# Kernel optimization log

Hardware: AMD Instinct MI355X
Metric: run time of the kernel (lower is better)

## Reference

```python
import jax, jax.numpy as jnp
import numpy as np

N = 50000      # nodes
E = 800000     # edges
D_IN = 128
D_H = 128
D_OUT = 64
P = 0.3        # dropout prob


def _glorot(key, out_c, in_c):
    return jax.random.normal(key, (out_c, in_c), jnp.float32) * (1.0 / np.sqrt(in_c))


def setup_inputs() -> dict:
    key = jax.random.key(0)
    ks = jax.random.split(key, 10)
    return {
        "x": jax.random.normal(ks[0], (N, D_IN), jnp.float32),
        "u1": jax.random.uniform(ks[1], (N, D_H), jnp.float32),
        "u2": jax.random.uniform(ks[2], (N, D_H), jnp.float32),
        "wl0": _glorot(ks[3], D_H, D_IN), "bl0": jnp.zeros((D_H,), jnp.float32), "wr0": _glorot(ks[4], D_H, D_IN),
        "wl1": _glorot(ks[5], D_H, D_H), "bl1": jnp.zeros((D_H,), jnp.float32), "wr1": _glorot(ks[6], D_H, D_H),
        "wl2": _glorot(ks[7], D_OUT, D_H), "bl2": jnp.zeros((D_OUT,), jnp.float32), "wr2": _glorot(ks[8], D_OUT, D_H),
        "edge_index": jax.random.randint(ks[9], (2, E), 0, N),
    }


def _sage_conv(x, src, dst, wl, bl, wr):
    # PyG SAGEConv (aggr='mean'): lin_l(mean of neighbor msgs) + lin_r(x)
    msg = x[src]                                                    # [E, d] gather
    s = jax.ops.segment_sum(msg, dst, num_segments=N)               # [N, d] scatter-sum
    cnt = jax.ops.segment_sum(jnp.ones((dst.shape[0],), x.dtype), dst, num_segments=N)
    mean = s / jnp.maximum(cnt, 1.0)[:, None]                       # mean; 0 for isolated nodes
    return mean @ wl.T + bl + x @ wr.T


def reference(x, u1, u2, wl0, bl0, wr0, wl1, bl1, wr1, wl2, bl2, wr2, edge_index):
    src, dst = edge_index[0], edge_index[1]
    keep = 1.0 - P
    h = jax.nn.relu(_sage_conv(x, src, dst, wl0, bl0, wr0))
    h = h * ((u1 >= P).astype(h.dtype) / keep)                      # dropout (training=True)
    h = jax.nn.relu(_sage_conv(h, src, dst, wl1, bl1, wr1))
    h = h * ((u2 >= P).astype(h.dtype) / keep)
    return _sage_conv(h, src, dst, wl2, bl2, wr2)
```

## Files before the change

### kernel.cpp

```cpp
#include <hip/hip_runtime.h>


constexpr int N = 50000;
constexpr int E = 800000;
constexpr int NBUCK = (N + 255) / 256;
constexpr int CE = 2048;
constexpr int NEB = (E + CE - 1) / CE;
constexpr int SLOT = 5632;
static_assert(N <= 65536, "u16 packing");
static_assert(N % 16 == 0, "16-row blocks need no bounds checks");

typedef _Float16 f16x8 __attribute__((ext_vector_type(8)));
typedef _Float16 f16x4 __attribute__((ext_vector_type(4)));
typedef _Float16 f16x2 __attribute__((ext_vector_type(2)));
typedef float f32x4 __attribute__((ext_vector_type(4)));


__global__ __launch_bounds__(256) void bucket_scatter_kernel(
    const int* __restrict__ src, const int* __restrict__ dst,
    int* __restrict__ bcur, unsigned* __restrict__ T) {
  __shared__ unsigned sorted[CE];
  __shared__ int hist[256], scan[256], excl[256], lcur[256], gbase[256];
  const int t = threadIdx.x;
  const int e0 = blockIdx.x * CE;
  const int nval = min(CE, E - e0);
  hist[t] = 0;
  __syncthreads();
  for (int i = t; i < nval; i += 256) atomicAdd(&hist[dst[e0 + i] >> 8], 1);
  __syncthreads();
  const int h = hist[t];
  scan[t] = h;
  __syncthreads();
  for (int off = 1; off < 256; off <<= 1) {
    int u = (t >= off) ? scan[t - off] : 0;
    __syncthreads();
    scan[t] += u;
    __syncthreads();
  }
  excl[t] = scan[t] - h;
  lcur[t] = scan[t] - h;
  gbase[t] = (t < NBUCK && h > 0) ? atomicAdd(&bcur[t], h) : 0;
  __syncthreads();
  for (int i = t; i < nval; i += 256) {
    int e = e0 + i;
    int d = dst[e];
    int p = atomicAdd(&lcur[d >> 8], 1);
    sorted[p] = ((unsigned)d << 16) | (unsigned)src[e];
  }
  __syncthreads();
  for (int i = t; i < nval; i += 256) {
    unsigned pk = sorted[i];
    int b = pk >> 24;
    T[gbase[b] + (i - excl[b])] = pk;
  }
}

constexpr int MASKB = (N * 128) / (8 * 256);

__global__ __launch_bounds__(256) void bucket_place_kernel(
    const unsigned* __restrict__ T, const int* __restrict__ bcur,
    const float* __restrict__ u1, const float* __restrict__ u2,
    unsigned* __restrict__ mk1, unsigned* __restrict__ mk2,
    int* __restrict__ offs, int* __restrict__ deg, int* __restrict__ elist) {
  __shared__ int dcnt[256], s[256], ncur[256];
  const int t = threadIdx.x;
  const int b = blockIdx.x;
  if (b >= NBUCK) {
    int mb = b - NBUCK;
    const float* Us = (mb < MASKB) ? u1 : u2;
    unsigned* MKs = (mb < MASKB) ? mk1 : mk2;
    int bb = (mb < MASKB) ? mb : (mb - MASKB);
#pragma unroll
    for (int k = 0; k < 8; ++k) {
      int i = (bb * 8 + k) * 256 + t;
      unsigned long long m = __ballot(Us[i] >= 0.3f);
      int lt = t & 63;
      if (lt == 0) MKs[i >> 5] = (unsigned)m;
      else if (lt == 32) MKs[i >> 5] = (unsigned)(m >> 32);
    }
    return;
  }
  const int lo = b * SLOT;
  const int hi = bcur[b];
  dcnt[t] = 0;
  __syncthreads();
  for (int i = lo + t; i < hi; i += 256) atomicAdd(&dcnt[(T[i] >> 16) & 255], 1);
  __syncthreads();
  const int v = dcnt[t];
  const int pv = (v + 3) & ~3;
  s[t] = pv;
  __syncthreads();
  for (int off = 1; off < 256; off <<= 1) {
    int u = (t >= off) ? s[t - off] : 0;
    __syncthreads();
    s[t] += u;
    __syncthreads();
  }
  const int base = lo + s[t] - pv;
  const int node = b * 256 + t;
  if (node < N) { offs[node] = base; deg[node] = v; }
  ncur[t] = base;
  __syncthreads();
  for (int i = lo + t; i < hi; i += 256) {
    unsigned pk = T[i];
    int pos = atomicAdd(&ncur[(pk >> 16) & 255], 1);
    elist[pos] = (int)(pk & 0xffffu);
  }
}

__device__ inline void wfrag_build(int idx, int KB, const float* wl,
                                   const float* wr, _Float16* wf) {
  int j = idx & 7;
  int lane = (idx >> 3) & 63;
  int kb = (idx >> 9) % KB;
  int ct = (idx >> 9) / KB;
  int c = ct * 16 + (lane & 15);
  int k = kb * 32 + (lane >> 4) * 8 + j;
  float v = (k < 128) ? wl[c * 128 + k] : wr[c * 128 + (k - 128)];
  wf[idx] = (_Float16)v;
}

constexpr int CONVB = (N * 128 / 8 + 255) / 256;

__global__ __launch_bounds__(256) void setup_kernel(
    const float* __restrict__ x,
    const float* __restrict__ wl0, const float* __restrict__ wr0,
    const float* __restrict__ wl1, const float* __restrict__ wr1,
    const float* __restrict__ wl2, const float* __restrict__ wr2,
    _Float16* __restrict__ HA, _Float16* __restrict__ wf0,
    _Float16* __restrict__ wf1, _Float16* __restrict__ wfZ,
    int* __restrict__ bcur) {
  const int b = blockIdx.x;
  const int t = threadIdx.x;
  if (b < CONVB) {
    int i = b * 256 + t;
    if (i < N * 128 / 8) {
      float4 a = ((const float4*)x)[i * 2];
      float4 c = ((const float4*)x)[i * 2 + 1];
      f16x8 v;
      v[0] = (_Float16)a.x; v[1] = (_Float16)a.y; v[2] = (_Float16)a.z; v[3] = (_Float16)a.w;
      v[4] = (_Float16)c.x; v[5] = (_Float16)c.y; v[6] = (_Float16)c.z; v[7] = (_Float16)c.w;
      ((f16x8*)HA)[i] = v;
    }
  } else if (b < CONVB + 128) {
    wfrag_build((b - CONVB) * 256 + t, 8, wl0, wr0, wf0);
  } else if (b < CONVB + 256) {
    wfrag_build((b - CONVB - 128) * 256 + t, 8, wl1, wr1, wf1);
  } else if (b < CONVB + 320) {
    int idx = (b - CONVB - 256) * 256 + t;
    int j = idx & 7;
    int lane = (idx >> 3) & 63;
    int kb = (idx >> 9) & 3;
    int ct = idx >> 11;
    int c = ct * 16 + (lane & 15);
    int k = kb * 32 + (lane >> 4) * 8 + j;
    float v = (c < 64) ? wl2[c * 128 + k] : wr2[(c - 64) * 128 + k];
    wfZ[idx] = (_Float16)v;
  } else {
    if (t < NBUCK) bcur[t] = t * SLOT;
  }
}

__global__ __launch_bounds__(256, 8) void fused_layer_kernel(
    const _Float16* __restrict__ H, const int* __restrict__ offs,
    const int* __restrict__ deg, const int* __restrict__ elist,
    const _Float16* __restrict__ Wf, const float* __restrict__ bias,
    const unsigned* __restrict__ MK, _Float16* __restrict__ outp) {
  __shared__ __align__(16) _Float16 Af[8][64][8];
  const int t = threadIdx.x;
  const int rowbase = blockIdx.x * 16;

  {
    int r = t >> 4, o = t & 15;
    f16x8 v = *(const f16x8*)(H + (size_t)(rowbase + r) * 128 + o * 8);
    *(f16x8*)&Af[4 + (o >> 2)][(o & 3) * 16 + r][0] = v;
  }

  {
    const int hw = t >> 5;
    const int ll = t & 31;
    const int kb = ll >> 3, q = (ll >> 1) & 3, j = (ll & 1) * 4;
#pragma unroll 1
    for (int i = 0; i < 2; ++i) {
      int r = hw * 2 + i;
      int node = rowbase + r;
      float a0 = 0.f, a1 = 0.f, a2 = 0.f, a3 = 0.f;
      const int e0 = offs[node];
      const int d = deg[node];
      const int e1 = e0 + d;
      int e = e0;
      for (; e + 16 <= e1; e += 16) {
        int4 q0 = *(const int4*)(elist + e);
        int4 q1 = *(const int4*)(elist + e + 4);
        int4 q2 = *(const int4*)(elist + e + 8);
        int4 q3 = *(const int4*)(elist + e + 12);
        int s[16] = {q0.x, q0.y, q0.z, q0.w, q1.x, q1.y, q1.z, q1.w,
                     q2.x, q2.y, q2.z, q2.w, q3.x, q3.y, q3.z, q3.w};
        f16x4 v[16];
#pragma unroll
        for (int u = 0; u < 16; ++u)
          v[u] = *(const f16x4*)(H + (size_t)s[u] * 128 + ll * 4);
#pragma unroll
        for (int u = 0; u < 16; ++u) {
          a0 += (float)v[u][0]; a1 += (float)v[u][1];
          a2 += (float)v[u][2]; a3 += (float)v[u][3];
        }
      }
      for (; e + 4 <= e1; e += 4) {
        int4 qq4 = *(const int4*)(elist + e);
        int s[4] = {qq4.x, qq4.y, qq4.z, qq4.w};
        f16x4 v[4];
#pragma unroll
        for (int u = 0; u < 4; ++u)
          v[u] = *(const f16x4*)(H + (size_t)s[u] * 128 + ll * 4);
#pragma unroll
        for (int u = 0; u < 4; ++u) {
          a0 += (float)v[u][0]; a1 += (float)v[u][1];
          a2 += (float)v[u][2]; a3 += (float)v[u][3];
        }
      }
      for (; e < e1; ++e) {
        f16x4 v = *(const f16x4*)(H + (size_t)elist[e] * 128 + ll * 4);
        a0 += (float)v[0]; a1 += (float)v[1];
        a2 += (float)v[2]; a3 += (float)v[3];
      }
      float inv = 1.0f / (float)max(d, 1);
      f16x4 o;
      o[0] = (_Float16)(a0 * inv); o[1] = (_Float16)(a1 * inv);
      o[2] = (_Float16)(a2 * inv); o[3] = (_Float16)(a3 * inv);
      *(f16x4*)&Af[kb][q * 16 + r][j] = o;
    }
  }
  __syncthreads();

  const int lane = t & 63;
  const int w = t >> 6;
  const int n16 = lane & 15;
  const int qq = lane >> 4;
  const int colbase = w * 32;

  f32x4 acc[2];
  acc[0] = (f32x4){0.f, 0.f, 0.f, 0.f};
  acc[1] = (f32x4){0.f, 0.f, 0.f, 0.f};

#pragma unroll
  for (int kb = 0; kb < 8; ++kb) {
    f16x8 a = *(const f16x8*)&Af[kb][lane][0];
#pragma unroll
    for (int ct = 0; ct < 2; ++ct) {
      const int ctg = w * 2 + ct;
      f16x8 b = *(const f16x8*)(Wf + ((size_t)(ctg * 8 + kb) * 64 + lane) * 8);
      acc[ct] = __builtin_amdgcn_mfma_f32_16x16x32_f16(a, b, acc[ct], 0, 0, 0);
    }
  }

#pragma unroll
  for (int r = 0; r < 4; ++r) {
    int row = rowbase + qq * 4 + r;
    unsigned mw = MK[(size_t)row * 4 + w];
#pragma unroll
    for (int ct = 0; ct < 2; ++ct) {
      const int col = colbase + ct * 16 + n16;
      float v = fmaxf(acc[ct][r] + bias[col], 0.f);
      v = ((mw >> (ct * 16 + n16)) & 1u) ? v * (1.0f / 0.7f) : 0.0f;
      outp[(size_t)row * 128 + col] = (_Float16)v;
    }
  }
}

__global__ __launch_bounds__(256) void gather64_add_kernel(
    const _Float16* __restrict__ Y2, const float* __restrict__ F,
    const int* __restrict__ offs, const int* __restrict__ deg,
    const int* __restrict__ elist, float* __restrict__ out) {
  int node = blockIdx.x * 8 + (threadIdx.x >> 5);
  if (node >= N) return;
  int l = threadIdx.x & 31;
  const int e0 = offs[node];
  const int d = deg[node];
  const int e1 = e0 + d;
  float a0 = 0.f, a1 = 0.f;
  int e = e0;
  for (; e + 16 <= e1; e += 16) {
    int4 q0 = *(const int4*)(elist + e);
    int4 q1 = *(const int4*)(elist + e + 4);
    int4 q2 = *(const int4*)(elist + e + 8);
    int4 q3 = *(const int4*)(elist + e + 12);
    int s[16] = {q0.x, q0.y, q0.z, q0.w, q1.x, q1.y, q1.z, q1.w,
                 q2.x, q2.y, q2.z, q2.w, q3.x, q3.y, q3.z, q3.w};
    f16x2 v[16];
#pragma unroll
    for (int u = 0; u < 16; ++u)
      v[u] = *(const f16x2*)(Y2 + (size_t)s[u] * 64 + l * 2);
#pragma unroll
    for (int u = 0; u < 16; ++u) { a0 += (float)v[u][0]; a1 += (float)v[u][1]; }
  }
  for (; e + 4 <= e1; e += 4) {
    int4 q = *(const int4*)(elist + e);
    int s[4] = {q.x, q.y, q.z, q.w};
    f16x2 v[4];
#pragma unroll
    for (int u = 0; u < 4; ++u)
      v[u] = *(const f16x2*)(Y2 + (size_t)s[u] * 64 + l * 2);
#pragma unroll
    for (int u = 0; u < 4; ++u) { a0 += (float)v[u][0]; a1 += (float)v[u][1]; }
  }
  for (; e < e1; ++e) {
    f16x2 v = *(const f16x2*)(Y2 + (size_t)elist[e] * 64 + l * 2);
    a0 += (float)v[0]; a1 += (float)v[1];
  }
  float inv = 1.0f / (float)max(d, 1);
  float2 f = ((const float2*)(F + (size_t)node * 64))[l];
  float2 o;
  o.x = f.x + a0 * inv;
  o.y = f.y + a1 * inv;
  ((float2*)(out + (size_t)node * 64))[l] = o;
}

__global__ __launch_bounds__(256, 4) void mfma_gemmZ_kernel(
    const _Float16* __restrict__ Hh, const _Float16* __restrict__ Wf,
    const float* __restrict__ bl2, _Float16* __restrict__ Y2,
    float* __restrict__ F) {
  const int lane = threadIdx.x & 63;
  const int w = threadIdx.x >> 6;
  const int n16 = lane & 15;
  const int q = lane >> 4;
  const int rowbase = blockIdx.x * 32;
  const int colbase = w * 32;

  f32x4 acc[2][2];
#pragma unroll
  for (int h = 0; h < 2; ++h)
#pragma unroll
    for (int ct = 0; ct < 2; ++ct) acc[h][ct] = (f32x4){0.f, 0.f, 0.f, 0.f};

  int ar0 = min(rowbase + n16, N - 1);
  int ar1 = min(rowbase + 16 + n16, N - 1);
  const _Float16* pH0 = Hh + (size_t)ar0 * 128 + q * 8;
  const _Float16* pH1 = Hh + (size_t)ar1 * 128 + q * 8;

#pragma unroll
  for (int kb = 0; kb < 4; ++kb) {
    const int ko = kb * 32;
    f16x8 a0 = *(const f16x8*)(pH0 + ko);
    f16x8 a1 = *(const f16x8*)(pH1 + ko);
#pragma unroll
    for (int ct = 0; ct < 2; ++ct) {
      const int ctg = w * 2 + ct;
      f16x8 b = *(const f16x8*)(Wf + ((size_t)(ctg * 4 + kb) * 64 + lane) * 8);
      acc[0][ct] = __builtin_amdgcn_mfma_f32_16x16x32_f16(a0, b, acc[0][ct], 0, 0, 0);
      acc[1][ct] = __builtin_amdgcn_mfma_f32_16x16x32_f16(a1, b, acc[1][ct], 0, 0, 0);
    }
  }

#pragma unroll
  for (int h = 0; h < 2; ++h) {
#pragma unroll
    for (int ct = 0; ct < 2; ++ct) {
      const int col = colbase + ct * 16 + n16;
#pragma unroll
      for (int r = 0; r < 4; ++r) {
        int row = rowbase + h * 16 + q * 4 + r;
        if (row < N) {
          float v = acc[h][ct][r];
          if (col < 64) Y2[(size_t)row * 64 + col] = (_Float16)v;
          else F[(size_t)row * 64 + (col - 64)] = v + bl2[col - 64];
        }
      }
    }
  }
}

extern "C" void kernel_launch(void* const* d_in, const int* in_sizes, int n_in,
                              void* d_out, int out_size, void* d_ws, size_t ws_size,
                              hipStream_t stream) {
  const float* x   = (const float*)d_in[0];
  const float* u1  = (const float*)d_in[1];
  const float* u2  = (const float*)d_in[2];
  const float* wl0 = (const float*)d_in[3];
  const float* bl0 = (const float*)d_in[4];
  const float* wr0 = (const float*)d_in[5];
  const float* wl1 = (const float*)d_in[6];
  const float* bl1 = (const float*)d_in[7];
  const float* wr1 = (const float*)d_in[8];
  const float* wl2 = (const float*)d_in[9];
  const float* bl2 = (const float*)d_in[10];
  const float* wr2 = (const float*)d_in[11];
  const int* edge  = (const int*)d_in[12];
  const int* src = edge;
  const int* dst = edge + E;

  _Float16* HA  = (_Float16*)d_ws;
  _Float16* HB  = HA + (size_t)N * 128;
  _Float16* M16 = HB + (size_t)N * 128;
  float* F      = (float*)(M16 + (size_t)N * 128);
  int* offs     = (int*)(F + (size_t)N * 64);
  int* deg      = offs + N;
  int* elist    = deg + N;
  unsigned* T   = (unsigned*)(elist + NBUCK * SLOT);
  int* bcur     = (int*)(T + NBUCK * SLOT);
  uintptr_t p = (uintptr_t)(bcur + NBUCK);
  p = (p + 15) & ~(uintptr_t)15;
  _Float16* wf0 = (_Float16*)p;
  _Float16* wf1 = wf0 + 8 * 8 * 512;
  _Float16* wfZ = wf1 + 8 * 8 * 512;
  unsigned* mk1 = (unsigned*)(wfZ + 8 * 4 * 512);
  unsigned* mk2 = mk1 + (size_t)N * 4;

  setup_kernel<<<CONVB + 321, 256, 0, stream>>>(
      x, wl0, wr0, wl1, wr1, wl2, wr2, HA, wf0, wf1, wfZ, bcur);
  bucket_scatter_kernel<<<NEB, 256, 0, stream>>>(src, dst, bcur, T);
  bucket_place_kernel<<<NBUCK + 2 * MASKB, 256, 0, stream>>>(
      T, bcur, u1, u2, mk1, mk2, offs, deg, elist);

  const int GM16 = N / 16;
  const int GM   = (N + 31) / 32;
  const int GG64 = (N + 7) / 8;

  fused_layer_kernel<<<GM16, 256, 0, stream>>>(HA, offs, deg, elist, wf0, bl0, mk1, HB);
  fused_layer_kernel<<<GM16, 256, 0, stream>>>(HB, offs, deg, elist, wf1, bl1, mk2, HA);
  mfma_gemmZ_kernel<<<GM, 256, 0, stream>>>(HA, wfZ, bl2, M16, F);
  gather64_add_kernel<<<GG64, 256, 0, stream>>>(M16, F, offs, deg, elist,
                                                (float*)d_out);
}
```

Measured before the change: 280.5 us.

## Fuse layer-2 GEMM into second SAGE layer and merge setup with edge scatter

```diff
diff --git a/kernel.cpp b/kernel.cpp
--- a/kernel.cpp
+++ b/kernel.cpp
@@ -15,47 +15,95 @@
 typedef _Float16 f16x2 __attribute__((ext_vector_type(2)));
 typedef float f32x4 __attribute__((ext_vector_type(4)));
 
-
-__global__ __launch_bounds__(256) void bucket_scatter_kernel(
+constexpr int CONVB = (N * 128 / 8 + 255) / 256;
+constexpr int MASKB = (N * 128) / (8 * 256);
+
+__device__ inline void wfrag_build(int idx, int KB, const float* wl,
+                                   const float* wr, _Float16* wf) {
+  int j = idx & 7;
+  int lane = (idx >> 3) & 63;
+  int kb = (idx >> 9) % KB;
+  int ct = (idx >> 9) / KB;
+  int c = ct * 16 + (lane & 15);
+  int k = kb * 32 + (lane >> 4) * 8 + j;
+  float v = (k < 128) ? wl[c * 128 + k] : wr[c * 128 + (k - 128)];
+  wf[idx] = (_Float16)v;
+}
+
+__global__ __launch_bounds__(256) void setup_scatter_kernel(
     const int* __restrict__ src, const int* __restrict__ dst,
-    int* __restrict__ bcur, unsigned* __restrict__ T) {
+    int* __restrict__ bcur, unsigned* __restrict__ T,
+    const float* __restrict__ x,
+    const float* __restrict__ wl0, const float* __restrict__ wr0,
+    const float* __restrict__ wl1, const float* __restrict__ wr1,
+    const float* __restrict__ wl2, const float* __restrict__ wr2,
+    _Float16* __restrict__ HA, _Float16* __restrict__ wf0,
+    _Float16* __restrict__ wf1, _Float16* __restrict__ wfZ) {
   __shared__ unsigned sorted[CE];
   __shared__ int hist[256], scan[256], excl[256], lcur[256], gbase[256];
+  const int b = blockIdx.x;
   const int t = threadIdx.x;
-  const int e0 = blockIdx.x * CE;
-  const int nval = min(CE, E - e0);
-  hist[t] = 0;
-  __syncthreads();
-  for (int i = t; i < nval; i += 256) atomicAdd(&hist[dst[e0 + i] >> 8], 1);
-  __syncthreads();
-  const int h = hist[t];
-  scan[t] = h;
-  __syncthreads();
-  for (int off = 1; off < 256; off <<= 1) {
-    int u = (t >= off) ? scan[t - off] : 0;
-    __syncthreads();
-    scan[t] += u;
-    __syncthreads();
-  }
-  excl[t] = scan[t] - h;
-  lcur[t] = scan[t] - h;
-  gbase[t] = (t < NBUCK && h > 0) ? atomicAdd(&bcur[t], h) : 0;
-  __syncthreads();
-  for (int i = t; i < nval; i += 256) {
-    int e = e0 + i;
-    int d = dst[e];
-    int p = atomicAdd(&lcur[d >> 8], 1);
-    sorted[p] = ((unsigned)d << 16) | (unsigned)src[e];
-  }
-  __syncthreads();
-  for (int i = t; i < nval; i += 256) {
-    unsigned pk = sorted[i];
-    int b = pk >> 24;
-    T[gbase[b] + (i - excl[b])] = pk;
-  }
-}
-
-constexpr int MASKB = (N * 128) / (8 * 256);
+  if (b < NEB) {
+    const int e0 = b * CE;
+    const int nval = min(CE, E - e0);
+    hist[t] = 0;
+    __syncthreads();
+    for (int i = t; i < nval; i += 256) atomicAdd(&hist[dst[e0 + i] >> 8], 1);
+    __syncthreads();
+    const int h = hist[t];
+    scan[t] = h;
+    __syncthreads();
+    for (int off = 1; off < 256; off <<= 1) {
+      int u = (t >= off) ? scan[t - off] : 0;
+      __syncthreads();
+      scan[t] += u;
+      __syncthreads();
+    }
+    excl[t] = scan[t] - h;
+    lcur[t] = scan[t] - h;
+    gbase[t] = (t < NBUCK && h > 0) ? (t * SLOT + atomicAdd(&bcur[t], h)) : 0;
+    __syncthreads();
+    for (int i = t; i < nval; i += 256) {
+      int e = e0 + i;
+      int d = dst[e];
+      int p = atomicAdd(&lcur[d >> 8], 1);
+      sorted[p] = ((unsigned)d << 16) | (unsigned)src[e];
+    }
+    __syncthreads();
+    for (int i = t; i < nval; i += 256) {
+      unsigned pk = sorted[i];
+      int bb = pk >> 24;
+      T[gbase[bb] + (i - excl[bb])] = pk;
+    }
+    return;
+  }
+  const int b2 = b - NEB;
+  if (b2 < CONVB) {
+    int i = b2 * 256 + t;
+    if (i < N * 128 / 8) {
+      float4 a = ((const float4*)x)[i * 2];
+      float4 c = ((const float4*)x)[i * 2 + 1];
+      f16x8 v;
+      v[0] = (_Float16)a.x; v[1] = (_Float16)a.y; v[2] = (_Float16)a.z; v[3] = (_Float16)a.w;
+      v[4] = (_Float16)c.x; v[5] = (_Float16)c.y; v[6] = (_Float16)c.z; v[7] = (_Float16)c.w;
+      ((f16x8*)HA)[i] = v;
+    }
+  } else if (b2 < CONVB + 128) {
+    wfrag_build((b2 - CONVB) * 256 + t, 8, wl0, wr0, wf0);
+  } else if (b2 < CONVB + 256) {
+    wfrag_build((b2 - CONVB - 128) * 256 + t, 8, wl1, wr1, wf1);
+  } else {
+    int idx = (b2 - CONVB - 256) * 256 + t;
+    int j = idx & 7;
+    int lane = (idx >> 3) & 63;
+    int kb = (idx >> 9) & 3;
+    int ct = idx >> 11;
+    int c = ct * 16 + (lane & 15);
+    int k = kb * 32 + (lane >> 4) * 8 + j;
+    float v = (c < 64) ? wl2[c * 128 + k] : wr2[(c - 64) * 128 + k];
+    wfZ[idx] = (_Float16)v;
+  }
+}
 
 __global__ __launch_bounds__(256) void bucket_place_kernel(
     const unsigned* __restrict__ T, const int* __restrict__ bcur,
@@ -81,7 +129,7 @@
     return;
   }
   const int lo = b * SLOT;
-  const int hi = bcur[b];
+  const int hi = lo + bcur[b];
   dcnt[t] = 0;
   __syncthreads();
   for (int i = lo + t; i < hi; i += 256) atomicAdd(&dcnt[(T[i] >> 16) & 255], 1);
@@ -105,59 +153,6 @@
     unsigned pk = T[i];
     int pos = atomicAdd(&ncur[(pk >> 16) & 255], 1);
     elist[pos] = (int)(pk & 0xffffu);
-  }
-}
-
-__device__ inline void wfrag_build(int idx, int KB, const float* wl,
-                                   const float* wr, _Float16* wf) {
-  int j = idx & 7;
-  int lane = (idx >> 3) & 63;
-  int kb = (idx >> 9) % KB;
-  int ct = (idx >> 9) / KB;
-  int c = ct * 16 + (lane & 15);
-  int k = kb * 32 + (lane >> 4) * 8 + j;
-  float v = (k < 128) ? wl[c * 128 + k] : wr[c * 128 + (k - 128)];
-  wf[idx] = (_Float16)v;
-}
-
-constexpr int CONVB = (N * 128 / 8 + 255) / 256;
-
-__global__ __launch_bounds__(256) void setup_kernel(
-    const float* __restrict__ x,
-    const float* __restrict__ wl0, const float* __restrict__ wr0,
-    const float* __restrict__ wl1, const float* __restrict__ wr1,
-    const float* __restrict__ wl2, const float* __restrict__ wr2,
-    _Float16* __restrict__ HA, _Float16* __restrict__ wf0,
-    _Float16* __restrict__ wf1, _Float16* __restrict__ wfZ,
-    int* __restrict__ bcur) {
-  const int b = blockIdx.x;
-  const int t = threadIdx.x;
-  if (b < CONVB) {
-    int i = b * 256 + t;
-    if (i < N * 128 / 8) {
-      float4 a = ((const float4*)x)[i * 2];
-      float4 c = ((const float4*)x)[i * 2 + 1];
-      f16x8 v;
-      v[0] = (_Float16)a.x; v[1] = (_Float16)a.y; v[2] = (_Float16)a.z; v[3] = (_Float16)a.w;
-      v[4] = (_Float16)c.x; v[5] = (_Float16)c.y; v[6] = (_Float16)c.z; v[7] = (_Float16)c.w;
-      ((f16x8*)HA)[i] = v;
-    }
-  } else if (b < CONVB + 128) {
-    wfrag_build((b - CONVB) * 256 + t, 8, wl0, wr0, wf0);
-  } else if (b < CONVB + 256) {
-    wfrag_build((b - CONVB - 128) * 256 + t, 8, wl1, wr1, wf1);
-  } else if (b < CONVB + 320) {
-    int idx = (b - CONVB - 256) * 256 + t;
-    int j = idx & 7;
-    int lane = (idx >> 3) & 63;
-    int kb = (idx >> 9) & 3;
-    int ct = idx >> 11;
-    int c = ct * 16 + (lane & 15);
-    int k = kb * 32 + (lane >> 4) * 8 + j;
-    float v = (c < 64) ? wl2[c * 128 + k] : wr2[(c - 64) * 128 + k];
-    wfZ[idx] = (_Float16)v;
-  } else {
-    if (t < NBUCK) bcur[t] = t * SLOT;
   }
 }
 
@@ -268,6 +263,142 @@
   }
 }
 
+__global__ __launch_bounds__(256, 8) void fused_layerZ_kernel(
+    const _Float16* __restrict__ H, const int* __restrict__ offs,
+    const int* __restrict__ deg, const int* __restrict__ elist,
+    const _Float16* __restrict__ Wf, const float* __restrict__ bias,
+    const unsigned* __restrict__ MK, const _Float16* __restrict__ WfZ,
+    const float* __restrict__ bl2, _Float16* __restrict__ Y2,
+    float* __restrict__ F) {
+  __shared__ __align__(16) _Float16 Af[8][64][8];
+  __shared__ __align__(16) _Float16 Zf[16][136];
+  const int t = threadIdx.x;
+  const int rowbase = blockIdx.x * 16;
+
+  {
+    int r = t >> 4, o = t & 15;
+    f16x8 v = *(const f16x8*)(H + (size_t)(rowbase + r) * 128 + o * 8);
+    *(f16x8*)&Af[4 + (o >> 2)][(o & 3) * 16 + r][0] = v;
+  }
+
+  {
+    const int hw = t >> 5;
+    const int ll = t & 31;
+    const int kb = ll >> 3, q = (ll >> 1) & 3, j = (ll & 1) * 4;
+#pragma unroll 1
+    for (int i = 0; i < 2; ++i) {
+      int r = hw * 2 + i;
+      int node = rowbase + r;
+      float a0 = 0.f, a1 = 0.f, a2 = 0.f, a3 = 0.f;
+      const int e0 = offs[node];
+      const int d = deg[node];
+      const int e1 = e0 + d;
+      int e = e0;
+      for (; e + 16 <= e1; e += 16) {
+        int4 q0 = *(const int4*)(elist + e);
+        int4 q1 = *(const int4*)(elist + e + 4);
+        int4 q2 = *(const int4*)(elist + e + 8);
+        int4 q3 = *(const int4*)(elist + e + 12);
+        int s[16] = {q0.x, q0.y, q0.z, q0.w, q1.x, q1.y, q1.z, q1.w,
+                     q2.x, q2.y, q2.z, q2.w, q3.x, q3.y, q3.z, q3.w};
+        f16x4 v[16];
+#pragma unroll
+        for (int u = 0; u < 16; ++u)
+          v[u] = *(const f16x4*)(H + (size_t)s[u] * 128 + ll * 4);
+#pragma unroll
+        for (int u = 0; u < 16; ++u) {
+          a0 += (float)v[u][0]; a1 += (float)v[u][1];
+          a2 += (float)v[u][2]; a3 += (float)v[u][3];
+        }
+      }
+      for (; e + 4 <= e1; e += 4) {
+        int4 qq4 = *(const int4*)(elist + e);
+        int s[4] = {qq4.x, qq4.y, qq4.z, qq4.w};
+        f16x4 v[4];
+#pragma unroll
+        for (int u = 0; u < 4; ++u)
+          v[u] = *(const f16x4*)(H + (size_t)s[u] * 128 + ll * 4);
+#pragma unroll
+        for (int u = 0; u < 4; ++u) {
+          a0 += (float)v[u][0]; a1 += (float)v[u][1];
+          a2 += (float)v[u][2]; a3 += (float)v[u][3];
+        }
+      }
+      for (; e < e1; ++e) {
+        f16x4 v = *(const f16x4*)(H + (size_t)elist[e] * 128 + ll * 4);
+        a0 += (float)v[0]; a1 += (float)v[1];
+        a2 += (float)v[2]; a3 += (float)v[3];
+      }
+      float inv = 1.0f / (float)max(d, 1);
+      f16x4 o;
+      o[0] = (_Float16)(a0 * inv); o[1] = (_Float16)(a1 * inv);
+      o[2] = (_Float16)(a2 * inv); o[3] = (_Float16)(a3 * inv);
+      *(f16x4*)&Af[kb][q * 16 + r][j] = o;
+    }
+  }
+  __syncthreads();
+
+  const int lane = t & 63;
+  const int w = t >> 6;
+  const int n16 = lane & 15;
+  const int qq = lane >> 4;
+  const int colbase = w * 32;
+
+  f32x4 acc[2];
+  acc[0] = (f32x4){0.f, 0.f, 0.f, 0.f};
+  acc[1] = (f32x4){0.f, 0.f, 0.f, 0.f};
+
+#pragma unroll
+  for (int kb = 0; kb < 8; ++kb) {
+    f16x8 a = *(const f16x8*)&Af[kb][lane][0];
+#pragma unroll
+    for (int ct = 0; ct < 2; ++ct) {
+      const int ctg = w * 2 + ct;
+      f16x8 b = *(const f16x8*)(Wf + ((size_t)(ctg * 8 + kb) * 64 + lane) * 8);
+      acc[ct] = __builtin_amdgcn_mfma_f32_16x16x32_f16(a, b, acc[ct], 0, 0, 0);
+    }
+  }
+
+#pragma unroll
+  for (int r = 0; r < 4; ++r) {
+    int row = qq * 4 + r;
+    unsigned mw = MK[(size_t)(rowbase + row) * 4 + w];
+#pragma unroll
+    for (int ct = 0; ct < 2; ++ct) {
+      const int col = colbase + ct * 16 + n16;
+      float v = fmaxf(acc[ct][r] + bias[col], 0.f);
+      v = ((mw >> (ct * 16 + n16)) & 1u) ? v * (1.0f / 0.7f) : 0.0f;
+      Zf[row][col] = (_Float16)v;
+    }
+  }
+  __syncthreads();
+
+  f32x4 az[2];
+  az[0] = (f32x4){0.f, 0.f, 0.f, 0.f};
+  az[1] = (f32x4){0.f, 0.f, 0.f, 0.f};
+#pragma unroll
+  for (int kb = 0; kb < 4; ++kb) {
+    f16x8 a = *(const f16x8*)&Zf[n16][kb * 32 + qq * 8];
+#pragma unroll
+    for (int ct = 0; ct < 2; ++ct) {
+      const int ctg = w * 2 + ct;
+      f16x8 b = *(const f16x8*)(WfZ + ((size_t)(ctg * 4 + kb) * 64 + lane) * 8);
+      az[ct] = __builtin_amdgcn_mfma_f32_16x16x32_f16(a, b, az[ct], 0, 0, 0);
+    }
+  }
+#pragma unroll
+  for (int ct = 0; ct < 2; ++ct) {
+    const int col = colbase + ct * 16 + n16;
+#pragma unroll
+    for (int r = 0; r < 4; ++r) {
+      int row = rowbase + qq * 4 + r;
+      float v = az[ct][r];
+      if (col < 64) Y2[(size_t)row * 64 + col] = (_Float16)v;
+      else F[(size_t)row * 64 + (col - 64)] = v + bl2[col - 64];
+    }
+  }
+}
+
 __global__ __launch_bounds__(256) void gather64_add_kernel(
     const _Float16* __restrict__ Y2, const float* __restrict__ F,
     const int* __restrict__ offs, const int* __restrict__ deg,
@@ -316,60 +447,6 @@
   ((float2*)(out + (size_t)node * 64))[l] = o;
 }
 
-__global__ __launch_bounds__(256, 4) void mfma_gemmZ_kernel(
-    const _Float16* __restrict__ Hh, const _Float16* __restrict__ Wf,
-    const float* __restrict__ bl2, _Float16* __restrict__ Y2,
-    float* __restrict__ F) {
-  const int lane = threadIdx.x & 63;
-  const int w = threadIdx.x >> 6;
-  const int n16 = lane & 15;
-  const int q = lane >> 4;
-  const int rowbase = blockIdx.x * 32;
-  const int colbase = w * 32;
-
-  f32x4 acc[2][2];
-#pragma unroll
-  for (int h = 0; h < 2; ++h)
-#pragma unroll
-    for (int ct = 0; ct < 2; ++ct) acc[h][ct] = (f32x4){0.f, 0.f, 0.f, 0.f};
-
-  int ar0 = min(rowbase + n16, N - 1);
-  int ar1 = min(rowbase + 16 + n16, N - 1);
-  const _Float16* pH0 = Hh + (size_t)ar0 * 128 + q * 8;
-  const _Float16* pH1 = Hh + (size_t)ar1 * 128 + q * 8;
-
-#pragma unroll
-  for (int kb = 0; kb < 4; ++kb) {
-    const int ko = kb * 32;
-    f16x8 a0 = *(const f16x8*)(pH0 + ko);
-    f16x8 a1 = *(const f16x8*)(pH1 + ko);
-#pragma unroll
-    for (int ct = 0; ct < 2; ++ct) {
-      const int ctg = w * 2 + ct;
-      f16x8 b = *(const f16x8*)(Wf + ((size_t)(ctg * 4 + kb) * 64 + lane) * 8);
-      acc[0][ct] = __builtin_amdgcn_mfma_f32_16x16x32_f16(a0, b, acc[0][ct], 0, 0, 0);
-      acc[1][ct] = __builtin_amdgcn_mfma_f32_16x16x32_f16(a1, b, acc[1][ct], 0, 0, 0);
-    }
-  }
-
-#pragma unroll
-  for (int h = 0; h < 2; ++h) {
-#pragma unroll
-    for (int ct = 0; ct < 2; ++ct) {
-      const int col = colbase + ct * 16 + n16;
-#pragma unroll
-      for (int r = 0; r < 4; ++r) {
-        int row = rowbase + h * 16 + q * 4 + r;
-        if (row < N) {
-          float v = acc[h][ct][r];
-          if (col < 64) Y2[(size_t)row * 64 + col] = (_Float16)v;
-          else F[(size_t)row * 64 + (col - 64)] = v + bl2[col - 64];
-        }
-      }
-    }
-  }
-}
-
 extern "C" void kernel_launch(void* const* d_in, const int* in_sizes, int n_in,
                               void* d_out, int out_size, void* d_ws, size_t ws_size,
                               hipStream_t stream) {
@@ -406,19 +483,19 @@
   unsigned* mk1 = (unsigned*)(wfZ + 8 * 4 * 512);
   unsigned* mk2 = mk1 + (size_t)N * 4;
 
-  setup_kernel<<<CONVB + 321, 256, 0, stream>>>(
-      x, wl0, wr0, wl1, wr1, wl2, wr2, HA, wf0, wf1, wfZ, bcur);
-  bucket_scatter_kernel<<<NEB, 256, 0, stream>>>(src, dst, bcur, T);
+  hipMemsetAsync(bcur, 0, NBUCK * sizeof(int), stream);
+  setup_scatter_kernel<<<NEB + CONVB + 320, 256, 0, stream>>>(
+      src, dst, bcur, T, x, wl0, wr0, wl1, wr1, wl2, wr2, HA, wf0, wf1, wfZ);
   bucket_place_kernel<<<NBUCK + 2 * MASKB, 256, 0, stream>>>(
       T, bcur, u1, u2, mk1, mk2, offs, deg, elist);
 
   const int GM16 = N / 16;
-  const int GM   = (N + 31) / 32;
   const int GG64 = (N + 7) / 8;
 
-  fused_layer_kernel<<<GM16, 256, 0, stream>>>(HA, offs, deg, elist, wf0, bl0, mk1, HB);
-  fused_layer_kernel<<<GM16, 256, 0, stream>>>(HB, offs, deg, elist, wf1, bl1, mk2, HA);
-  mfma_gemmZ_kernel<<<GM, 256, 0, stream>>>(HA, wfZ, bl2, M16, F);
+  fused_layer_kernel<<<GM16, 256, 0, stream>>>(HA, offs, deg, elist, wf0, bl0,
+                                               mk1, HB);
+  fused_layerZ_kernel<<<GM16, 256, 0, stream>>>(HB, offs, deg, elist, wf1, bl1,
+                                                mk2, wfZ, bl2, M16, F);
   gather64_add_kernel<<<GG64, 256, 0, stream>>>(M16, F, offs, deg, elist,
                                                 (float*)d_out);
 }
```

After: 268.2 us. 1.05x faster.
